# Kernel optimization log

Measured on AMD Instinct MI355X. Metric: run time of the kernel, lower is better.

The kernel has to match this reference:

```python
import jax, jax.numpy as jnp
import numpy as np

N, P, S, M, K, L = 1024, 4, 12, 64, 16, 8
SNR = 20.0
PWR = 1.0
DECAY = L // 2  # Channel is built with decay = L // 2
MK = M + K
SMK = (S + 1) * MK
LOUT = L + SMK - 1  # full linear-convolution length


def _to_c(x):
    return x[..., 0] + 1j * x[..., 1]


def _to_r(x):
    return jnp.stack([x.real, x.imag], axis=-1)


def setup_inputs() -> dict:
    key = jax.random.key(0)
    k1, k2, k3, k4 = jax.random.split(key, 4)
    return {
        "x": jax.random.normal(k1, (N, P, S, M, 2), jnp.float32),
        "pilot_raw": jax.random.normal(k2, (N, P, 1, M, 2), jnp.float32),
        "cof_unit": jax.random.normal(k3, (N, P, L, 2), jnp.float32),
        "noise_unit": jax.random.normal(k4, (N, P, S + 1, MK, 2), jnp.float32),
    }


def reference(x, pilot_raw, cof_unit, noise_unit):
    # --- pilot: Normalize -> ifft -> add CP (done once in torch __init__) ---
    power = jnp.mean(pilot_raw ** 2, axis=(-2, -1), keepdims=True)  # (N,P,1,1,1)
    alpha = jnp.sqrt(PWR / 2) / jnp.sqrt(power)
    pilot = jnp.fft.ifft(_to_c(alpha * pilot_raw), axis=-1)          # (N,P,1,M) complex
    pilot = jnp.concatenate([pilot[..., -K:], pilot], axis=-1)        # add CP -> (N,P,1,MK)

    # --- payload: ifft -> add CP ---
    xt = jnp.fft.ifft(_to_c(x), axis=-1)                              # (N,P,S,M)
    xt = jnp.concatenate([xt[..., -K:], xt], axis=-1)                 # (N,P,S,MK)

    sig = jnp.concatenate([pilot, xt], axis=2).reshape(N, P, SMK)     # serialized complex signal

    # --- channel taps: sqrt(power_profile/2) * randn (cof is None path) ---
    prof = jnp.exp(-jnp.arange(L, dtype=jnp.float32) / DECAY)
    prof = prof / jnp.sum(prof)
    cof = _to_c(jnp.sqrt(prof / 2)[:, None] * cof_unit)               # (N,P,L) complex

    cof_true = jnp.concatenate([cof, jnp.zeros((N, P, M - L), cof.dtype)], axis=-1)
    H_true = jnp.fft.fft(cof_true, axis=-1)                           # (N,P,M)

    # --- L-tap linear convolution (equivalent to dense Toeplitz bmm) ---
    s_pad = jnp.pad(sig, ((0, 0), (0, 0), (L - 1, L - 1)))            # (N,P,SMK+2(L-1))
    y = jnp.zeros((N, P, LOUT), sig.dtype)
    for t in range(L):  # fixed small tap count
        y = y + cof[:, :, t:t + 1] * s_pad[:, :, L - 1 - t: L - 1 - t + LOUT]

    out = y[:, :, :SMK].reshape(N, P, S + 1, MK)

    # --- AWGN (default SNR path, isTest=False) ---
    noise_pwr = PWR / (M * 10.0 ** (0.1 * SNR))
    out = out + np.sqrt(noise_pwr / 2) * _to_c(noise_unit)

    # --- split pilot/signal, remove CP, FFT back to frequency domain ---
    info_pilot = jnp.fft.fft(out[:, :, 0:1, K:], axis=-1)             # (N,P,1,M)
    info_sig = jnp.fft.fft(out[:, :, 1:, K:], axis=-1)                # (N,P,S,M)

    return (_to_r(info_pilot), _to_r(info_sig), _to_r(H_true),
            jnp.float32(noise_pwr))
```

## Files before the change

### kernel.cpp

```cpp
#include <hip/hip_runtime.h>
#include <math.h>

#define NN   1024
#define PP   4
#define SS   12
#define MM   64
#define KK   16
#define LL   8
#define MKK  80
#define NSYM 13
#define SMK  1040

#define OFF_PILOT  0
#define OFF_SIG    524288
#define OFF_H      6815744
#define OFF_SCALAR 7340032

#define NOISE_PWR   1.5625e-4f
#define NOISE_SCALE 8.8388347648318447e-3f
#define INV_2SUM    0.1279105570f

__device__ __forceinline__ float2 shflx(float2 v, int mask) {
    return make_float2(__shfl_xor(v.x, mask), __shfl_xor(v.y, mask));
}


template<int CONJ, int NS>
__device__ __forceinline__ void fft64_dif(float2* v, const float2* tw, const float* sgn) {
    #pragma unroll
    for (int s = 5; s >= 0; --s) {
        float2 o[NS];
        #pragma unroll
        for (int j = 0; j < NS; ++j) o[j] = shflx(v[j], 1 << s);
        const float sg = sgn[s], tx = tw[s].x;
        const float ty = CONJ ? -tw[s].y : tw[s].y;
        #pragma unroll
        for (int j = 0; j < NS; ++j) {
            float dx = fmaf(sg, v[j].x, o[j].x);
            float dy = fmaf(sg, v[j].y, o[j].y);
            v[j].x = dx * tx - dy * ty;
            v[j].y = dx * ty + dy * tx;
        }
    }
}

template<int NS>
__device__ __forceinline__ void fft64_dit(float2* v, const float2* tw, const float* sgn) {
    #pragma unroll
    for (int s = 0; s < 6; ++s) {
        const float sg = sgn[s], tx = tw[s].x, ty = tw[s].y;
        float ax[NS], ay[NS];
        #pragma unroll
        for (int j = 0; j < NS; ++j) {
            ax[j] = v[j].x * tx - v[j].y * ty;
            ay[j] = v[j].x * ty + v[j].y * tx;
        }
        float2 o[NS];
        #pragma unroll
        for (int j = 0; j < NS; ++j) o[j] = shflx(make_float2(ax[j], ay[j]), 1 << s);
        #pragma unroll
        for (int j = 0; j < NS; ++j) {
            v[j].x = fmaf(sg, ax[j], o[j].x);
            v[j].y = fmaf(sg, ay[j], o[j].y);
        }
    }
}

__global__ __launch_bounds__(256) void ofdm_kernel(
    const float2* __restrict__ x,
    const float2* __restrict__ pilot_raw,
    const float2* __restrict__ cof_unit,
    const float2* __restrict__ noise_unit,
    float2* __restrict__ out_pilot,
    float2* __restrict__ out_sig,
    float2* __restrict__ out_H,
    float*  __restrict__ out_scalar)
{
    const int b    = blockIdx.x;
    const int tid  = threadIdx.x;
    const int wid  = tid >> 6;
    const int lane = tid & 63;

    __shared__ float2 sig[SMK];

    const float2* xb = x          + (size_t)b * (SS*MM);
    const float2* pb = pilot_raw  + (size_t)b * MM;
    const float2* cb = cof_unit   + (size_t)b * LL;
    const float2* nb = noise_unit + (size_t)b * (NSYM*MKK);

    float2 tw[6];
    float  sgn[6];
    #pragma unroll
    for (int s = 0; s < 6; ++s) {
        const int h = 1 << s;
        const bool up = (lane & h) != 0;
        sgn[s] = up ? -1.0f : 1.0f;
        float ang = -6.2831853071795864769f * (float)(lane & (h - 1)) / (float)(2 * h);
        float sn, cs;
        __sincosf(ang, &sn, &cs);
        tw[s] = up ? make_float2(cs, sn) : make_float2(1.0f, 0.0f);
    }
    const int rb = (int)(__brev((unsigned)lane) >> 26);

    float2 cof[LL];
    #pragma unroll
    for (int t = 0; t < LL; ++t) {
        float sc = sqrtf(__expf(-(float)t * 0.25f) * INV_2SUM);
        float2 u = cb[t];
        cof[t] = make_float2(sc * u.x, sc * u.y);
    }

    auto store_sig = [&](int sym, float2 vv) {
        vv.x *= (1.0f / 64.0f);
        vv.y *= (1.0f / 64.0f);
        sig[sym * MKK + KK + rb] = vv;
        if (rb >= MM - KK) sig[sym * MKK + rb - (MM - KK)] = vv;
    };

    if (wid == 0) {
        float2 v[4];
        float2 pv = pb[lane];
        v[1] = xb[3 * MM + lane];
        v[2] = xb[7 * MM + lane];
        v[3] = xb[11 * MM + lane];
        float ssq = pv.x * pv.x + pv.y * pv.y;
        #pragma unroll
        for (int off = 32; off > 0; off >>= 1)
            ssq += __shfl_xor(ssq, off);
        float alpha = sqrtf(64.0f / ssq);
        v[0] = make_float2(alpha * pv.x, alpha * pv.y);
        fft64_dif<1, 4>(v, tw, sgn);
        store_sig(0, v[0]); store_sig(4, v[1]); store_sig(8, v[2]); store_sig(12, v[3]);
    } else {
        float2 v[3];
        v[0] = xb[(wid - 1) * MM + lane];
        v[1] = xb[(wid + 3) * MM + lane];
        v[2] = xb[(wid + 7) * MM + lane];
        fft64_dif<1, 3>(v, tw, sgn);
        store_sig(wid, v[0]); store_sig(wid + 4, v[1]); store_sig(wid + 8, v[2]);
    }

    __syncthreads();

    auto fir = [&](int sym) -> float2 {
        const int pos = sym * MKK + KK + rb;
        float2 nu = nb[pos];
        float2 acc = make_float2(NOISE_SCALE * nu.x, NOISE_SCALE * nu.y);
        #pragma unroll
        for (int t = 0; t < LL; ++t) {
            float2 c = cof[t];
            float2 s2 = sig[pos - t];
            acc.x += c.x * s2.x - c.y * s2.y;
            acc.y += c.x * s2.y + c.y * s2.x;
        }
        return acc;
    };

    const size_t ob = (size_t)b * MM;
    const size_t osb = (size_t)b * (SS * MM);

    if (wid <= 1) {
        float2 v[4];
        v[0] = fir(wid);
        v[1] = fir(wid + 4);
        v[2] = fir(wid + 8);
        if (wid == 0) {
            v[3] = fir(12);
        } else {
            float2 h = make_float2(0.0f, 0.0f);
            if (rb < LL) {
                float sc = sqrtf(__expf(-(float)rb * 0.25f) * INV_2SUM);
                float2 u = cb[rb];
                h = make_float2(sc * u.x, sc * u.y);
            }
            v[3] = h;
        }
        fft64_dit<4>(v, tw, sgn);
        if (wid == 0) {
            out_pilot[ob + lane]            = v[0];
            out_sig[osb + 3 * MM + lane]    = v[1];
            out_sig[osb + 7 * MM + lane]    = v[2];
            out_sig[osb + 11 * MM + lane]   = v[3];
        } else {
            out_sig[osb + 0 * MM + lane]    = v[0];
            out_sig[osb + 4 * MM + lane]    = v[1];
            out_sig[osb + 8 * MM + lane]    = v[2];
            out_H[ob + lane]                = v[3];
        }
    } else {
        float2 v[3];
        v[0] = fir(wid);
        v[1] = fir(wid + 4);
        v[2] = fir(wid + 8);
        fft64_dit<3>(v, tw, sgn);
        out_sig[osb + (wid - 1) * MM + lane] = v[0];
        out_sig[osb + (wid + 3) * MM + lane] = v[1];
        out_sig[osb + (wid + 7) * MM + lane] = v[2];
    }

    if (b == 0 && tid == 0) out_scalar[0] = NOISE_PWR;
}

extern "C" void kernel_launch(void* const* d_in, const int* in_sizes, int n_in,
                              void* d_out, int out_size, void* d_ws, size_t ws_size,
                              hipStream_t stream) {
    const float2* x  = (const float2*)d_in[0];
    const float2* pr = (const float2*)d_in[1];
    const float2* cu = (const float2*)d_in[2];
    const float2* nu = (const float2*)d_in[3];

    float* out = (float*)d_out;
    float2* out_pilot = (float2*)(out + OFF_PILOT);
    float2* out_sig   = (float2*)(out + OFF_SIG);
    float2* out_H     = (float2*)(out + OFF_H);
    float*  out_sc    = out + OFF_SCALAR;

    ofdm_kernel<<<dim3(NN*PP), dim3(256), 0, stream>>>(
        x, pr, cu, nu, out_pilot, out_sig, out_H, out_sc);
}
```

Measured before the change: 120.7 us.

## Replace IFFT+FIR+FFT with frequency-domain channel multiply plus noise FFT

New measurement: 106.1 us. 12.1% less time.

```diff
diff --git a/kernel.cpp b/kernel.cpp
--- a/kernel.cpp
+++ b/kernel.cpp
@@ -9,7 +9,6 @@
 #define LL   8
 #define MKK  80
 #define NSYM 13
-#define SMK  1040
 
 #define OFF_PILOT  0
 #define OFF_SIG    524288
@@ -20,28 +19,12 @@
 #define NOISE_SCALE 8.8388347648318447e-3f
 #define INV_2SUM    0.1279105570f
 
+
 __device__ __forceinline__ float2 shflx(float2 v, int mask) {
     return make_float2(__shfl_xor(v.x, mask), __shfl_xor(v.y, mask));
 }
-
-
-template<int CONJ, int NS>
-__device__ __forceinline__ void fft64_dif(float2* v, const float2* tw, const float* sgn) {
-    #pragma unroll
-    for (int s = 5; s >= 0; --s) {
-        float2 o[NS];
-        #pragma unroll
-        for (int j = 0; j < NS; ++j) o[j] = shflx(v[j], 1 << s);
-        const float sg = sgn[s], tx = tw[s].x;
-        const float ty = CONJ ? -tw[s].y : tw[s].y;
-        #pragma unroll
-        for (int j = 0; j < NS; ++j) {
-            float dx = fmaf(sg, v[j].x, o[j].x);
-            float dy = fmaf(sg, v[j].y, o[j].y);
-            v[j].x = dx * tx - dy * ty;
-            v[j].y = dx * ty + dy * tx;
-        }
-    }
+__device__ __forceinline__ float2 cmul(float2 a, float2 b) {
+    return make_float2(a.x*b.x - a.y*b.y, a.x*b.y + a.y*b.x);
 }
 
 template<int NS>
@@ -81,12 +64,20 @@
     const int wid  = tid >> 6;
     const int lane = tid & 63;
 
-    __shared__ float2 sig[SMK];
-
     const float2* xb = x          + (size_t)b * (SS*MM);
     const float2* pb = pilot_raw  + (size_t)b * MM;
     const float2* cb = cof_unit   + (size_t)b * LL;
     const float2* nb = noise_unit + (size_t)b * (NSYM*MKK);
+
+    const int rb = (int)(__brev((unsigned)lane) >> 26);
+
+    float2 cof[LL];
+    #pragma unroll
+    for (int t = 0; t < LL; ++t) {
+        float2 u = cb[t];
+        float sc = sqrtf(__expf(-(float)t * 0.25f) * INV_2SUM);
+        cof[t] = make_float2(sc * u.x, sc * u.y);
+    }
 
     float2 tw[6];
     float  sgn[6];
@@ -100,102 +91,68 @@
         __sincosf(ang, &sn, &cs);
         tw[s] = up ? make_float2(cs, sn) : make_float2(1.0f, 0.0f);
     }
-    const int rb = (int)(__brev((unsigned)lane) >> 26);
 
-    float2 cof[LL];
+    float sn, cs;
+    __sincosf(-0.0981747704246810387f * (float)lane, &sn, &cs);
+    const float2 w = make_float2(cs, sn);
+    float2 H = cof[LL - 1];
     #pragma unroll
-    for (int t = 0; t < LL; ++t) {
-        float sc = sqrtf(__expf(-(float)t * 0.25f) * INV_2SUM);
-        float2 u = cb[t];
-        cof[t] = make_float2(sc * u.x, sc * u.y);
+    for (int l = LL - 2; l >= 0; --l) {
+        float2 Hw = cmul(H, w);
+        H = make_float2(Hw.x + cof[l].x, Hw.y + cof[l].y);
     }
 
-    auto store_sig = [&](int sym, float2 vv) {
-        vv.x *= (1.0f / 64.0f);
-        vv.y *= (1.0f / 64.0f);
-        sig[sym * MKK + KK + rb] = vv;
-        if (rb >= MM - KK) sig[sym * MKK + rb - (MM - KK)] = vv;
-    };
+    const size_t ob  = (size_t)b * MM;
+    const size_t osb = (size_t)b * (SS * MM);
+
+    if (wid == 1) out_H[ob + lane] = H;
 
     if (wid == 0) {
-        float2 v[4];
+        float2 nv[4];
+        nv[0] = nb[ 0*MKK + KK + rb];
+        nv[1] = nb[ 4*MKK + KK + rb];
+        nv[2] = nb[ 8*MKK + KK + rb];
+        nv[3] = nb[12*MKK + KK + rb];
         float2 pv = pb[lane];
-        v[1] = xb[3 * MM + lane];
-        v[2] = xb[7 * MM + lane];
-        v[3] = xb[11 * MM + lane];
+        float2 X1 = xb[ 3*MM + lane];
+        float2 X2 = xb[ 7*MM + lane];
+        float2 X3 = xb[11*MM + lane];
+        #pragma unroll
+        for (int j = 0; j < 4; ++j) {
+            nv[j].x *= NOISE_SCALE; nv[j].y *= NOISE_SCALE;
+        }
+        fft64_dit<4>(nv, tw, sgn);
+
         float ssq = pv.x * pv.x + pv.y * pv.y;
         #pragma unroll
         for (int off = 32; off > 0; off >>= 1)
             ssq += __shfl_xor(ssq, off);
         float alpha = sqrtf(64.0f / ssq);
-        v[0] = make_float2(alpha * pv.x, alpha * pv.y);
-        fft64_dif<1, 4>(v, tw, sgn);
-        store_sig(0, v[0]); store_sig(4, v[1]); store_sig(8, v[2]); store_sig(12, v[3]);
+        float2 X0 = make_float2(alpha * pv.x, alpha * pv.y);
+
+        float2 o0 = cmul(H, X0), o1 = cmul(H, X1), o2 = cmul(H, X2), o3 = cmul(H, X3);
+        out_pilot[ob + lane]          = make_float2(o0.x + nv[0].x, o0.y + nv[0].y);
+        out_sig[osb +  3*MM + lane]   = make_float2(o1.x + nv[1].x, o1.y + nv[1].y);
+        out_sig[osb +  7*MM + lane]   = make_float2(o2.x + nv[2].x, o2.y + nv[2].y);
+        out_sig[osb + 11*MM + lane]   = make_float2(o3.x + nv[3].x, o3.y + nv[3].y);
     } else {
-        float2 v[3];
-        v[0] = xb[(wid - 1) * MM + lane];
-        v[1] = xb[(wid + 3) * MM + lane];
-        v[2] = xb[(wid + 7) * MM + lane];
-        fft64_dif<1, 3>(v, tw, sgn);
-        store_sig(wid, v[0]); store_sig(wid + 4, v[1]); store_sig(wid + 8, v[2]);
-    }
+        float2 nv[3];
+        nv[0] = nb[(wid    ) * MKK + KK + rb];
+        nv[1] = nb[(wid + 4) * MKK + KK + rb];
+        nv[2] = nb[(wid + 8) * MKK + KK + rb];
+        float2 X0 = xb[(wid - 1) * MM + lane];
+        float2 X1 = xb[(wid + 3) * MM + lane];
+        float2 X2 = xb[(wid + 7) * MM + lane];
+        #pragma unroll
+        for (int j = 0; j < 3; ++j) {
+            nv[j].x *= NOISE_SCALE; nv[j].y *= NOISE_SCALE;
+        }
+        fft64_dit<3>(nv, tw, sgn);
 
-    __syncthreads();
-
-    auto fir = [&](int sym) -> float2 {
-        const int pos = sym * MKK + KK + rb;
-        float2 nu = nb[pos];
-        float2 acc = make_float2(NOISE_SCALE * nu.x, NOISE_SCALE * nu.y);
-        #pragma unroll
-        for (int t = 0; t < LL; ++t) {
-            float2 c = cof[t];
-            float2 s2 = sig[pos - t];
-            acc.x += c.x * s2.x - c.y * s2.y;
-            acc.y += c.x * s2.y + c.y * s2.x;
-        }
-        return acc;
-    };
-
-    const size_t ob = (size_t)b * MM;
-    const size_t osb = (size_t)b * (SS * MM);
-
-    if (wid <= 1) {
-        float2 v[4];
-        v[0] = fir(wid);
-        v[1] = fir(wid + 4);
-        v[2] = fir(wid + 8);
-        if (wid == 0) {
-            v[3] = fir(12);
-        } else {
-            float2 h = make_float2(0.0f, 0.0f);
-            if (rb < LL) {
-                float sc = sqrtf(__expf(-(float)rb * 0.25f) * INV_2SUM);
-                float2 u = cb[rb];
-                h = make_float2(sc * u.x, sc * u.y);
-            }
-            v[3] = h;
-        }
-        fft64_dit<4>(v, tw, sgn);
-        if (wid == 0) {
-            out_pilot[ob + lane]            = v[0];
-            out_sig[osb + 3 * MM + lane]    = v[1];
-            out_sig[osb + 7 * MM + lane]    = v[2];
-            out_sig[osb + 11 * MM + lane]   = v[3];
-        } else {
-            out_sig[osb + 0 * MM + lane]    = v[0];
-            out_sig[osb + 4 * MM + lane]    = v[1];
-            out_sig[osb + 8 * MM + lane]    = v[2];
-            out_H[ob + lane]                = v[3];
-        }
-    } else {
-        float2 v[3];
-        v[0] = fir(wid);
-        v[1] = fir(wid + 4);
-        v[2] = fir(wid + 8);
-        fft64_dit<3>(v, tw, sgn);
-        out_sig[osb + (wid - 1) * MM + lane] = v[0];
-        out_sig[osb + (wid + 3) * MM + lane] = v[1];
-        out_sig[osb + (wid + 7) * MM + lane] = v[2];
+        float2 o0 = cmul(H, X0), o1 = cmul(H, X1), o2 = cmul(H, X2);
+        out_sig[osb + (wid - 1) * MM + lane] = make_float2(o0.x + nv[0].x, o0.y + nv[0].y);
+        out_sig[osb + (wid + 3) * MM + lane] = make_float2(o1.x + nv[1].x, o1.y + nv[1].y);
+        out_sig[osb + (wid + 7) * MM + lane] = make_float2(o2.x + nv[2].x, o2.y + nv[2].y);
     }
 
     if (b == 0 && tid == 0) out_scalar[0] = NOISE_PWR;
```
